# Optimization experiments

Hardware: AMD Instinct MI355X
Metric: run time of the kernel (lower is better)

Reference implementation:

```python
import jax, jax.numpy as jnp
import numpy as np

B, T, C, H, HD = 2, 2048, 1024, 16, 64
EPS = 1e-6

def rmsnorm(x):
    return x * jax.lax.rsqrt(jnp.mean(x * x, axis=-1, keepdims=True) + EPS)

def rotary_cos_sin(seq_len, hd):
    inv_freq = 1.0 / (10000.0 ** (jnp.arange(0, hd, 2, dtype=jnp.float32) / hd))
    freqs = jnp.arange(seq_len, dtype=jnp.float32)[:, None] * inv_freq[None, :]  # [T, hd/2]
    return jnp.cos(freqs)[None, :, None, :], jnp.sin(freqs)[None, :, None, :]

def apply_rotary(x, cos, sin):
    x1, x2 = x[..., : HD // 2], x[..., HD // 2 :]
    return jnp.concatenate([x1 * cos + x2 * sin, -x1 * sin + x2 * cos], axis=-1)


def setup_inputs() -> dict:
    key = jax.random.key(0)
    ks = jax.random.split(key, 8)
    return {
        "x": jax.random.normal(ks[0], (B, T, C), jnp.float32),
        "w_qkv": jax.random.normal(ks[1], (3 * C, C), jnp.float32) * 0.02,
        "w_out": jax.random.normal(ks[2], (C, C), jnp.float32) * 0.02,
        "hyp_curvature": jax.random.uniform(ks[3], (1, H, 1, 1), jnp.float32, 0.5, 1.5),
        "w_uv": jax.random.normal(ks[4], (8 * C, C), jnp.float32) * 0.02,
        "b_uv": jnp.zeros((8 * C,), jnp.float32),
        "w_mlp_out": jax.random.normal(ks[5], (C, 4 * C), jnp.float32) * 0.02,
        "b_mlp_out": jnp.zeros((C,), jnp.float32),
    }


def reference(x, w_qkv, w_out, hyp_curvature, w_uv, b_uv, w_mlp_out, b_mlp_out):
    # --- pre-norm (euc/hyp branch uses rms_norm) ---
    h = rmsnorm(x)
    # --- QKV projection ---
    qkv = h @ w_qkv.T  # [B,T,3C]
    q, k, v = jnp.split(qkv, 3, axis=-1)
    q = q.reshape(B, T, H, HD)
    k = k.reshape(B, T, H, HD)
    v = v.reshape(B, T, H, HD)
    # --- RoPE ---
    cos, sin = rotary_cos_sin(T, HD)
    q = apply_rotary(q, cos, sin)
    k = apply_rotary(k, cos, sin)
    # [B,H,T,HD]
    q = jnp.transpose(q, (0, 2, 1, 3))
    k = jnp.transpose(k, (0, 2, 1, 3))
    v = jnp.transpose(v, (0, 2, 1, 3))
    # --- hyperbolic (Lorentz) attention ---
    kc = hyp_curvature  # [1,H,1,1], positive per-head curvature
    q0 = jnp.sqrt(kc + jnp.sum(q * q, axis=-1, keepdims=True))  # time coord [B,H,T,1]
    k0 = jnp.sqrt(kc + jnp.sum(k * k, axis=-1, keepdims=True))
    # Lorentz inner product <u,v>_L = -u0*v0 + u.v  -> [B,H,T,S]
    lorentz = jnp.einsum("bhtd,bhsd->bhts", q, k) - q0 * jnp.swapaxes(k0, -1, -2)
    dis = jnp.sqrt(kc) * jnp.arccosh(jnp.maximum(-lorentz / kc, 1.0 + EPS))
    causal = jnp.tril(jnp.ones((T, T), dtype=bool))
    scores = jnp.where(causal, -dis, -jnp.inf)  # hyp_attn_weight='neg_dis'
    attn_w = jax.nn.softmax(scores, axis=-1)
    attn = jnp.einsum("bhts,bhsd->bhtd", attn_w, v)
    attn = jnp.transpose(attn, (0, 2, 1, 3)).reshape(B, T, C)
    x = x + attn @ w_out.T
    # --- SwiGLU MLP with pre rms_norm ---
    h = rmsnorm(x)
    uv = h @ w_uv.T + b_uv
    u, vg = jnp.split(uv, 2, axis=-1)
    h_mlp = (u * jax.nn.silu(vg)) @ w_mlp_out.T + b_mlp_out
    return x + h_mlp
```

## Files before the change

kernel.cpp:

```cpp
#include <hip/hip_runtime.h>
#include <cstdint>
#include <cmath>

typedef __bf16 bf16;
typedef __attribute__((ext_vector_type(8))) __bf16 bf16x8;
typedef __attribute__((ext_vector_type(4))) __bf16 bf16x4;
typedef __attribute__((ext_vector_type(2))) __bf16 bf16x2;
typedef __attribute__((ext_vector_type(4))) float f32x4;

constexpr int B_ = 2, T_ = 2048, C_ = 1024, H_ = 16, HD_ = 64;
constexpr int M_ = B_ * T_;

#define EXP2F(x) __builtin_amdgcn_exp2f(x)
#define LOG2F(x) __builtin_amdgcn_logf(x)
#define SQRTF(x) __builtin_amdgcn_sqrtf(x)
#define RCPF(x)  __builtin_amdgcn_rcpf(x)

__device__ __forceinline__ void gld16(const void* g, void* l) {
  __builtin_amdgcn_global_load_lds((const __attribute__((address_space(1))) void*)g,
                                   (__attribute__((address_space(3))) void*)l, 16, 0, 0);
}

__global__ __launch_bounds__(256) void cast_all_kernel(const float* __restrict__ s0,
                                                       const float* __restrict__ s1,
                                                       const float* __restrict__ s2,
                                                       const float* __restrict__ s3,
                                                       const float* __restrict__ s4,
                                                       bf16* __restrict__ d0,
                                                       bf16* __restrict__ d1,
                                                       bf16* __restrict__ d2,
                                                       bf16* __restrict__ d3,
                                                       float* __restrict__ d4) {
  size_t gid = (size_t)blockIdx.x * 256 + threadIdx.x;
  if (gid >= 786432 + 262144 + 2097152 + 1048576) {
    size_t g4 = gid - (786432 + 262144 + 2097152 + 1048576);
    if (g4 >= 2048) return;
    int r = (int)(g4 * 4);
    int dr;
    if (r < 4096) { int blk = r >> 6, i = r & 63; dr = blk * 128 + i; }
    else { int j = r - 4096; int blk = j >> 6, i = j & 63; dr = blk * 128 + 64 + i; }
    *(f32x4*)(d4 + dr) = *(const f32x4*)(s4 + r);
    return;
  }
  const float* src;
  bf16* dst;
  size_t dstoff;
  if (gid < 786432) { src = s0; dst = d0; dstoff = gid * 4; }
  else if (gid < 786432 + 262144) { gid -= 786432; src = s1; dst = d1; dstoff = gid * 4; }
  else if (gid < 786432 + 262144 + 2097152) {
    gid -= 786432 + 262144; src = s2; dst = d2;
    size_t elem = gid * 4;
    int r = (int)(elem >> 10), c = (int)(elem & 1023);
    int dr;
    if (r < 4096) { int blk = r >> 6, i = r & 63; dr = blk * 128 + i; }
    else { int j = r - 4096; int blk = j >> 6, i = j & 63; dr = blk * 128 + 64 + i; }
    dstoff = ((size_t)dr << 10) | (size_t)c;
  }
  else { gid -= 786432 + 262144 + 2097152; src = s3; dst = d3; dstoff = gid * 4; }
  f32x4 v = *(const f32x4*)(src + gid * 4);
  bf16x4 o;
  o[0] = (bf16)v[0]; o[1] = (bf16)v[1]; o[2] = (bf16)v[2]; o[3] = (bf16)v[3];
  *(bf16x4*)(dst + dstoff) = o;
}

template <int MODE, typename OutT>
__global__ __launch_bounds__(256) void gemm_bt(const bf16* __restrict__ A,
                                               const bf16* __restrict__ Bw,
                                               OutT* __restrict__ Cmat,
                                               const float* __restrict__ bias,
                                               const float* __restrict__ R,
                                               int M, int N, int K, int lda) {
  __shared__ __align__(16) bf16 shmem[4 * 128 * 32];
  bf16* const AlsH[2] = { &shmem[0], &shmem[4096] };
  bf16* const BlsH[2] = { &shmem[2 * 4096], &shmem[3 * 4096] };
  const int tid  = threadIdx.x;
  const int wave = tid >> 6;
  const int lane = tid & 63;
  const int quad = lane >> 4;
  const int l16  = lane & 15;
  const int bm = blockIdx.x * 128;
  const int bn = blockIdx.y * 128;
  const int wm = (wave & 1) * 64;
  const int wn = (wave >> 1) * 64;
  const int wn2 = (wave >> 1) * 32;
  const int srow   = lane >> 2;
  const int schunk = lane & 3;

  f32x4 acc[4][4];
#pragma unroll
  for (int i = 0; i < 4; i++)
#pragma unroll
    for (int j = 0; j < 4; j++) acc[i][j] = f32x4{0.f, 0.f, 0.f, 0.f};

  const bf16* Ag = A  + (size_t)(bm + wave * 32 + srow) * lda + schunk * 8;
  const bf16* Bg = Bw + (size_t)(bn + wave * 32 + srow) * K   + schunk * 8;
  bf16* AlsW0 = AlsH[0] + (wave * 32) * 32;
  bf16* AlsW1 = AlsH[1] + (wave * 32) * 32;
  bf16* BlsW0 = BlsH[0] + (wave * 32) * 32;
  bf16* BlsW1 = BlsH[1] + (wave * 32) * 32;

  for (int k0 = 0; k0 < K; k0 += 64) {
    gld16(Ag + k0,                         AlsW0);
    gld16(Ag + k0 + (size_t)16 * lda,      AlsW0 + 16 * 32);
    gld16(Ag + k0 + 32,                    AlsW1);
    gld16(Ag + k0 + 32 + (size_t)16 * lda, AlsW1 + 16 * 32);
    gld16(Bg + k0,                         BlsW0);
    gld16(Bg + k0 + (size_t)16 * K,        BlsW0 + 16 * 32);
    gld16(Bg + k0 + 32,                    BlsW1);
    gld16(Bg + k0 + 32 + (size_t)16 * K,   BlsW1 + 16 * 32);
    __syncthreads();

#pragma unroll
    for (int hh = 0; hh < 2; hh++) {
      bf16x8 af[4], bfr[4];
#pragma unroll
      for (int mt = 0; mt < 4; mt++)
        af[mt] = *(const bf16x8*)&AlsH[hh][(wm + mt * 16 + l16) * 32 + quad * 8];
#pragma unroll
      for (int nt = 0; nt < 4; nt++) {
        const int cb = (MODE == 4)
                         ? ((nt < 2) ? (wn2 + nt * 16) : (64 + wn2 + (nt - 2) * 16))
                         : (wn + nt * 16);
        bfr[nt] = *(const bf16x8*)&BlsH[hh][(cb + l16) * 32 + quad * 8];
      }
#pragma unroll
      for (int mt = 0; mt < 4; mt++)
#pragma unroll
        for (int nt = 0; nt < 4; nt++)
          acc[mt][nt] = __builtin_amdgcn_mfma_f32_16x16x32_bf16(af[mt], bfr[nt], acc[mt][nt], 0, 0, 0);
    }
    __syncthreads();
  }

  if (MODE != 4) {
#pragma unroll
    for (int mt = 0; mt < 4; mt++) {
      const int row = bm + wm + mt * 16 + quad * 4;
#pragma unroll
      for (int nt = 0; nt < 4; nt++) {
        const int col = bn + wn + nt * 16 + l16;
        float bval = 0.f;
        if (MODE & 2) bval = bias[col];
#pragma unroll
        for (int r = 0; r < 4; r++) {
          float v = acc[mt][nt][r] + bval;
          if (MODE & 1) v += R[(size_t)(row + r) * N + col];
          Cmat[(size_t)(row + r) * N + col] = (OutT)v;
        }
      }
    }
  } else {
    const int colg0 = (bn >> 1) + wn2;
#pragma unroll
    for (int mt = 0; mt < 4; mt++) {
      const int row = bm + wm + mt * 16 + quad * 4;
#pragma unroll
      for (int ntl = 0; ntl < 2; ntl++) {
        const float bu = bias[bn + wn2 + ntl * 16 + l16];
        const float bv = bias[bn + 64 + wn2 + ntl * 16 + l16];
        const int col = colg0 + ntl * 16 + l16;
#pragma unroll
        for (int r = 0; r < 4; r++) {
          float u = acc[mt][ntl][r] + bu;
          float v = acc[mt][ntl + 2][r] + bv;
          float sig = RCPF(1.f + EXP2F(-v * 1.44269504f));
          Cmat[(size_t)(row + r) * N + col] = (OutT)(u * v * sig);
        }
      }
    }
  }
}

__global__ __launch_bounds__(256) void rmsnorm_kernel(const float* __restrict__ X,
                                                      bf16* __restrict__ O) {
  const int row = blockIdx.x;
  const int tid = threadIdx.x;
  const int wave = tid >> 6;
  f32x4 v = *(const f32x4*)(X + (size_t)row * C_ + tid * 4);
  float s = v[0] * v[0] + v[1] * v[1] + v[2] * v[2] + v[3] * v[3];
#pragma unroll
  for (int off = 32; off >= 1; off >>= 1) s += __shfl_xor(s, off);
  __shared__ float wsum[4];
  __shared__ float scale_sh;
  if ((tid & 63) == 0) wsum[wave] = s;
  __syncthreads();
  if (tid == 0)
    scale_sh = rsqrtf((wsum[0] + wsum[1] + wsum[2] + wsum[3]) * (1.f / (float)C_) + 1e-6f);
  __syncthreads();
  const float sc = scale_sh;
  bf16x4 o;
  o[0] = (bf16)(v[0] * sc); o[1] = (bf16)(v[1] * sc);
  o[2] = (bf16)(v[2] * sc); o[3] = (bf16)(v[3] * sc);
  *(bf16x4*)(O + (size_t)row * C_ + tid * 4) = o;
}

__global__ __launch_bounds__(256) void rotary_kernel(bf16* __restrict__ qkv,
                                                     const float* __restrict__ kcb,
                                                     float* __restrict__ q0b,
                                                     float* __restrict__ k0b) {
  const int wid  = blockIdx.x * 4 + (threadIdx.x >> 6);
  const int lane = threadIdx.x & 63;
  const int b = wid >> 15;
  const int rem = wid & 32767;
  const int t = rem >> 4;
  const int h = rem & 15;
  const int i = lane & 31;
  const float invf = expf(-((float)i / 32.f) * 9.210340371976184f);
  const float ang = (float)t * invf;
  const float cx = cosf(ang), sx = sinf(ang);
  const float kc = kcb[h];
  bf16* qp = qkv + (size_t)(b * T_ + t) * 3072 + h * 64;

#pragma unroll
  for (int which = 0; which < 2; which++) {
    bf16* p = qp + which * 1024;
    float x1 = (float)p[i];
    float x2 = (float)p[i + 32];
    float o = (lane < 32) ? (x1 * cx + x2 * sx) : (x2 * cx - x1 * sx);
    float ss = o * o;
#pragma unroll
    for (int off = 32; off >= 1; off >>= 1) ss += __shfl_xor(ss, off);
    p[lane] = (bf16)o;
    if (lane == 0) {
      float* dst = which == 0 ? q0b : k0b;
      dst[(size_t)(b * H_ + h) * T_ + t] = SQRTF(kc + ss);
    }
  }
}

__global__ __launch_bounds__(256) void attn_kernel(const bf16* __restrict__ qkv,
                                                   const float* __restrict__ q0b,
                                                   const float* __restrict__ k0b,
                                                   const float* __restrict__ kcb,
                                                   bf16* __restrict__ outp) {
  __shared__ __align__(16) bf16 Kls[2][64][72];
  __shared__ __align__(16) bf16 Vt[2][64][68];
  __shared__ __align__(16) bf16 Pls[4][16 * 36];
  __shared__ float k0s[2][64];

  const int tid = threadIdx.x;
  const int wave = tid >> 6, lane = tid & 63;
  const int quad = lane >> 4, l16 = lane & 15;
  const int bh = blockIdx.x;
  const int b = bh >> 4, h = bh & 15;

  const float kc = kcb[h];
  const float inv_kc = 1.f / kc;
  const float sqkc = SQRTF(kc);
  const int sp = tid & 31, dq = tid >> 5;
  bf16* Pl = Pls[wave];
  const float* q0base = q0b + (size_t)(b * H_ + h) * T_;
  const float* k0base = k0b + (size_t)(b * H_ + h) * T_;

  const int ty = 31 - (int)blockIdx.y;
  const int t0 = ty * 64;
  const int tb = t0 + wave * 16;
  const int nIter = ty + 1;

  const bf16* qrow = qkv + (size_t)(b * T_ + tb + l16) * 3072 + h * 64;
  bf16x8 aq0 = *(const bf16x8*)(qrow + quad * 8);
  bf16x8 aq1 = *(const bf16x8*)(qrow + 32 + quad * 8);
  float q0r[4];
#pragma unroll
  for (int r = 0; r < 4; r++) q0r[r] = q0base[tb + quad * 4 + r];

  f32x4 o[4];
#pragma unroll
  for (int dt = 0; dt < 4; dt++) o[dt] = f32x4{0.f, 0.f, 0.f, 0.f};
  float lrow[4] = {0.f, 0.f, 0.f, 0.f};

  const bf16* kvbase = qkv + (size_t)b * T_ * 3072 + 1024 + h * 64 + dq * 8;
  bf16x8 kv_a = *(const bf16x8*)(kvbase + (size_t)(2 * sp) * 3072);
  bf16x8 kv_b = *(const bf16x8*)(kvbase + (size_t)(2 * sp + 1) * 3072);
  bf16x8 vv_a = *(const bf16x8*)(kvbase + (size_t)(2 * sp) * 3072 + 1024);
  bf16x8 vv_b = *(const bf16x8*)(kvbase + (size_t)(2 * sp + 1) * 3072 + 1024);
  float k0v = (tid < 64) ? k0base[tid] : 0.f;

  for (int it = 0; it < nIter; ++it) {
    const int s0 = it * 64;
    const int buf = it & 1;
    *(bf16x8*)&Kls[buf][2 * sp][dq * 8]     = kv_a;
    *(bf16x8*)&Kls[buf][2 * sp + 1][dq * 8] = kv_b;
#pragma unroll
    for (int i2 = 0; i2 < 8; i2++) {
      bf16x2 pr;
      pr[0] = vv_a[i2];
      pr[1] = vv_b[i2];
      *(bf16x2*)&Vt[buf][dq * 8 + i2][2 * sp] = pr;
    }
    if (tid < 64) k0s[buf][tid] = k0v;
    __syncthreads();

    const int s0n = (it + 1 < nIter) ? s0 + 64 : s0;
    kv_a = *(const bf16x8*)(kvbase + (size_t)(s0n + 2 * sp) * 3072);
    kv_b = *(const bf16x8*)(kvbase + (size_t)(s0n + 2 * sp + 1) * 3072);
    vv_a = *(const bf16x8*)(kvbase + (size_t)(s0n + 2 * sp) * 3072 + 1024);
    vv_b = *(const bf16x8*)(kvbase + (size_t)(s0n + 2 * sp + 1) * 3072 + 1024);
    if (tid < 64) k0v = k0base[s0n + tid];

    f32x4 sc[4];
#pragma unroll
    for (int nt = 0; nt < 4; nt++) {
      sc[nt] = f32x4{0.f, 0.f, 0.f, 0.f};
      bf16x8 b0 = *(const bf16x8*)&Kls[buf][nt * 16 + l16][quad * 8];
      bf16x8 b1 = *(const bf16x8*)&Kls[buf][nt * 16 + l16][32 + quad * 8];
      sc[nt] = __builtin_amdgcn_mfma_f32_16x16x32_bf16(aq0, b0, sc[nt], 0, 0, 0);
      sc[nt] = __builtin_amdgcn_mfma_f32_16x16x32_bf16(aq1, b1, sc[nt], 0, 0, 0);
    }

    bf16x8 ap[2];
#pragma unroll
    for (int ck = 0; ck < 2; ck++) {
#pragma unroll
      for (int ntl = 0; ntl < 2; ntl++) {
        const int nt = ck * 2 + ntl;
        const float k0c = k0s[buf][nt * 16 + l16];
        const int s = s0 + nt * 16 + l16;
#pragma unroll
        for (int r = 0; r < 4; r++) {
          const int t = tb + quad * 4 + r;
          float lor = sc[nt][r] - q0r[r] * k0c;
          float ratio = fmaxf(-lor * inv_kc, 1.f + 1e-6f);
          float wv = ratio + SQRTF(ratio * ratio - 1.f);
          float p = EXP2F(-sqkc * LOG2F(wv));
          p = (s <= t) ? p : 0.f;
          lrow[r] += p;
          Pl[(quad * 4 + r) * 36 + ntl * 16 + l16] = (bf16)p;
        }
      }
      ap[ck] = *(const bf16x8*)&Pl[l16 * 36 + quad * 8];
    }
#pragma unroll
    for (int dt = 0; dt < 4; dt++) {
      bf16x8 bv0 = *(const bf16x8*)&Vt[buf][dt * 16 + l16][quad * 8];
      bf16x8 bv1 = *(const bf16x8*)&Vt[buf][dt * 16 + l16][32 + quad * 8];
      o[dt] = __builtin_amdgcn_mfma_f32_16x16x32_bf16(ap[0], bv0, o[dt], 0, 0, 0);
      o[dt] = __builtin_amdgcn_mfma_f32_16x16x32_bf16(ap[1], bv1, o[dt], 0, 0, 0);
    }
  }

#pragma unroll
  for (int r = 0; r < 4; r++) {
#pragma unroll
    for (int off = 1; off <= 8; off <<= 1) lrow[r] += __shfl_xor(lrow[r], off);
  }
#pragma unroll
  for (int r = 0; r < 4; r++) {
    const float invl = RCPF(lrow[r]);
    const int t = tb + quad * 4 + r;
#pragma unroll
    for (int dt = 0; dt < 4; dt++) {
      float val = o[dt][r] * invl;
      outp[(size_t)(b * T_ + t) * C_ + h * 64 + dt * 16 + l16] = (bf16)val;
    }
  }
}

extern "C" void kernel_launch(void* const* d_in, const int* in_sizes, int n_in,
                              void* d_out, int out_size, void* d_ws, size_t ws_size,
                              hipStream_t stream) {
  const float* x      = (const float*)d_in[0];
  const float* w_qkv  = (const float*)d_in[1];
  const float* w_out  = (const float*)d_in[2];
  const float* kcb    = (const float*)d_in[3];
  const float* w_uv   = (const float*)d_in[4];
  const float* b_uv   = (const float*)d_in[5];
  const float* w_mlp  = (const float*)d_in[6];
  const float* b_mlp  = (const float*)d_in[7];
  float* out = (float*)d_out;

  const size_t MB = 1024ull * 1024ull;
  char* w = (char*)d_ws;
  bf16*  wqkv_b  = (bf16*)(w + 0);
  bf16*  wout_b  = (bf16*)(w + 6 * MB);
  bf16*  wuv_p   = (bf16*)(w + 8 * MB);
  bf16*  wmlp_b  = (bf16*)(w + 24 * MB);
  bf16*  hbuf    = (bf16*)(w + 32 * MB);
  bf16*  qkvbuf  = (bf16*)(w + 40 * MB);
  bf16*  attnbuf = (bf16*)(w + 64 * MB);
  bf16*  gbuf    = (bf16*)(w + 40 * MB);
  float* x2buf   = (float*)(w + 72 * MB);
  float* q0b     = (float*)(w + 88 * MB);
  float* k0b     = (float*)(w + 88 * MB + 256 * 1024);
  float* biasp   = (float*)(w + 88 * MB + 512 * 1024);

  const int total4 = 786432 + 262144 + 2097152 + 1048576 + 2048;
  cast_all_kernel<<<(total4 + 255) / 256, 256, 0, stream>>>(
      w_qkv, w_out, w_uv, w_mlp, b_uv, wqkv_b, wout_b, wuv_p, wmlp_b, biasp);

  rmsnorm_kernel<<<M_, 256, 0, stream>>>(x, hbuf);
  gemm_bt<0, bf16><<<dim3(M_ / 128, 3072 / 128), 256, 0, stream>>>(
      hbuf, wqkv_b, qkvbuf, nullptr, nullptr, M_, 3072, 1024, 1024);
  rotary_kernel<<<(B_ * T_ * H_) / 4, 256, 0, stream>>>(qkvbuf, kcb, q0b, k0b);
  attn_kernel<<<dim3(B_ * H_, 32), 256, 0, stream>>>(qkvbuf, q0b, k0b, kcb, attnbuf);
  gemm_bt<1, float><<<dim3(M_ / 128, 1024 / 128), 256, 0, stream>>>(
      attnbuf, wout_b, x2buf, nullptr, x, M_, 1024, 1024, 1024);
  rmsnorm_kernel<<<M_, 256, 0, stream>>>(x2buf, hbuf);
  gemm_bt<4, bf16><<<dim3(M_ / 128, 8192 / 128), 256, 0, stream>>>(
      hbuf, wuv_p, gbuf, biasp, nullptr, M_, 4096, 1024, 1024);
  gemm_bt<3, float><<<dim3(M_ / 128, 1024 / 128), 256, 0, stream>>>(
      gbuf, wmlp_b, out, b_mlp, x2buf, M_, 1024, 4096, 4096);
}
```

Baseline: 437.7 us.

## Use 512-thread attention blocks with split K/V loaders and smaller GEMM M-tiles

```diff
diff --git a/kernel.cpp b/kernel.cpp
--- a/kernel.cpp
+++ b/kernel.cpp
@@ -63,58 +63,59 @@
   *(bf16x4*)(dst + dstoff) = o;
 }
 
-template <int MODE, typename OutT>
+template <int MODE, typename OutT, int BM = 128>
 __global__ __launch_bounds__(256) void gemm_bt(const bf16* __restrict__ A,
                                                const bf16* __restrict__ Bw,
                                                OutT* __restrict__ Cmat,
                                                const float* __restrict__ bias,
                                                const float* __restrict__ R,
                                                int M, int N, int K, int lda) {
-  __shared__ __align__(16) bf16 shmem[4 * 128 * 32];
-  bf16* const AlsH[2] = { &shmem[0], &shmem[4096] };
-  bf16* const BlsH[2] = { &shmem[2 * 4096], &shmem[3 * 4096] };
+  __shared__ __align__(16) bf16 shmem[(2 * BM + 2 * 128) * 32];
+  bf16* const AlsH[2] = { &shmem[0], &shmem[BM * 32] };
+  bf16* const BlsH[2] = { &shmem[2 * BM * 32], &shmem[2 * BM * 32 + 4096] };
   const int tid  = threadIdx.x;
   const int wave = tid >> 6;
   const int lane = tid & 63;
   const int quad = lane >> 4;
   const int l16  = lane & 15;
-  const int bm = blockIdx.x * 128;
+  const int bm = blockIdx.x * BM;
   const int bn = blockIdx.y * 128;
-  const int wm = (wave & 1) * 64;
+  const int wm = (wave & 1) * (BM / 2);
   const int wn = (wave >> 1) * 64;
   const int wn2 = (wave >> 1) * 32;
   const int srow   = lane >> 2;
   const int schunk = lane & 3;
-
-  f32x4 acc[4][4];
-#pragma unroll
-  for (int i = 0; i < 4; i++)
+  constexpr int MT = BM / 32;
+
+  f32x4 acc[MT][4];
+#pragma unroll
+  for (int i = 0; i < MT; i++)
 #pragma unroll
     for (int j = 0; j < 4; j++) acc[i][j] = f32x4{0.f, 0.f, 0.f, 0.f};
 
-  const bf16* Ag = A  + (size_t)(bm + wave * 32 + srow) * lda + schunk * 8;
+  const bf16* Ag = A  + (size_t)(bm + wave * (BM / 4) + srow) * lda + schunk * 8;
   const bf16* Bg = Bw + (size_t)(bn + wave * 32 + srow) * K   + schunk * 8;
-  bf16* AlsW0 = AlsH[0] + (wave * 32) * 32;
-  bf16* AlsW1 = AlsH[1] + (wave * 32) * 32;
+  bf16* AlsW0 = AlsH[0] + (wave * (BM / 4)) * 32;
+  bf16* AlsW1 = AlsH[1] + (wave * (BM / 4)) * 32;
   bf16* BlsW0 = BlsH[0] + (wave * 32) * 32;
   bf16* BlsW1 = BlsH[1] + (wave * 32) * 32;
 
   for (int k0 = 0; k0 < K; k0 += 64) {
-    gld16(Ag + k0,                         AlsW0);
-    gld16(Ag + k0 + (size_t)16 * lda,      AlsW0 + 16 * 32);
-    gld16(Ag + k0 + 32,                    AlsW1);
-    gld16(Ag + k0 + 32 + (size_t)16 * lda, AlsW1 + 16 * 32);
-    gld16(Bg + k0,                         BlsW0);
-    gld16(Bg + k0 + (size_t)16 * K,        BlsW0 + 16 * 32);
-    gld16(Bg + k0 + 32,                    BlsW1);
-    gld16(Bg + k0 + 32 + (size_t)16 * K,   BlsW1 + 16 * 32);
+    gld16(Ag + k0, AlsW0);
+    if (BM == 128) gld16(Ag + k0 + (size_t)16 * lda, AlsW0 + 16 * 32);
+    gld16(Ag + k0 + 32, AlsW1);
+    if (BM == 128) gld16(Ag + k0 + 32 + (size_t)16 * lda, AlsW1 + 16 * 32);
+    gld16(Bg + k0,                       BlsW0);
+    gld16(Bg + k0 + (size_t)16 * K,      BlsW0 + 16 * 32);
+    gld16(Bg + k0 + 32,                  BlsW1);
+    gld16(Bg + k0 + 32 + (size_t)16 * K, BlsW1 + 16 * 32);
     __syncthreads();
 
 #pragma unroll
     for (int hh = 0; hh < 2; hh++) {
-      bf16x8 af[4], bfr[4];
-#pragma unroll
-      for (int mt = 0; mt < 4; mt++)
+      bf16x8 af[MT], bfr[4];
+#pragma unroll
+      for (int mt = 0; mt < MT; mt++)
         af[mt] = *(const bf16x8*)&AlsH[hh][(wm + mt * 16 + l16) * 32 + quad * 8];
 #pragma unroll
       for (int nt = 0; nt < 4; nt++) {
@@ -124,7 +125,7 @@
         bfr[nt] = *(const bf16x8*)&BlsH[hh][(cb + l16) * 32 + quad * 8];
       }
 #pragma unroll
-      for (int mt = 0; mt < 4; mt++)
+      for (int mt = 0; mt < MT; mt++)
 #pragma unroll
         for (int nt = 0; nt < 4; nt++)
           acc[mt][nt] = __builtin_amdgcn_mfma_f32_16x16x32_bf16(af[mt], bfr[nt], acc[mt][nt], 0, 0, 0);
@@ -134,7 +135,7 @@
 
   if (MODE != 4) {
 #pragma unroll
-    for (int mt = 0; mt < 4; mt++) {
+    for (int mt = 0; mt < MT; mt++) {
       const int row = bm + wm + mt * 16 + quad * 4;
 #pragma unroll
       for (int nt = 0; nt < 4; nt++) {
@@ -152,7 +153,7 @@
   } else {
     const int colg0 = (bn >> 1) + wn2;
 #pragma unroll
-    for (int mt = 0; mt < 4; mt++) {
+    for (int mt = 0; mt < MT; mt++) {
       const int row = bm + wm + mt * 16 + quad * 4;
 #pragma unroll
       for (int ntl = 0; ntl < 2; ntl++) {
@@ -228,14 +229,14 @@
   }
 }
 
-__global__ __launch_bounds__(256) void attn_kernel(const bf16* __restrict__ qkv,
+__global__ __launch_bounds__(512) void attn_kernel(const bf16* __restrict__ qkv,
                                                    const float* __restrict__ q0b,
                                                    const float* __restrict__ k0b,
                                                    const float* __restrict__ kcb,
                                                    bf16* __restrict__ outp) {
   __shared__ __align__(16) bf16 Kls[2][64][72];
   __shared__ __align__(16) bf16 Vt[2][64][68];
-  __shared__ __align__(16) bf16 Pls[4][16 * 36];
+  __shared__ __align__(16) bf16 Pls[8][16 * 36];
   __shared__ float k0s[2][64];
 
   const int tid = threadIdx.x;
@@ -247,15 +248,17 @@
   const float kc = kcb[h];
   const float inv_kc = 1.f / kc;
   const float sqkc = SQRTF(kc);
-  const int sp = tid & 31, dq = tid >> 5;
+  const int role = tid >> 8;
+  const int st = tid & 255;
+  const int sp = st & 31, dq = st >> 5;
   bf16* Pl = Pls[wave];
   const float* q0base = q0b + (size_t)(b * H_ + h) * T_;
   const float* k0base = k0b + (size_t)(b * H_ + h) * T_;
 
-  const int ty = 31 - (int)blockIdx.y;
-  const int t0 = ty * 64;
+  const int ty = 15 - (int)blockIdx.y;
+  const int t0 = ty * 128;
   const int tb = t0 + wave * 16;
-  const int nIter = ty + 1;
+  const int nIter = 2 * ty + 2;
 
   const bf16* qrow = qkv + (size_t)(b * T_ + tb + l16) * 3072 + h * 64;
   bf16x8 aq0 = *(const bf16x8*)(qrow + quad * 8);
@@ -269,73 +272,74 @@
   for (int dt = 0; dt < 4; dt++) o[dt] = f32x4{0.f, 0.f, 0.f, 0.f};
   float lrow[4] = {0.f, 0.f, 0.f, 0.f};
 
-  const bf16* kvbase = qkv + (size_t)b * T_ * 3072 + 1024 + h * 64 + dq * 8;
-  bf16x8 kv_a = *(const bf16x8*)(kvbase + (size_t)(2 * sp) * 3072);
-  bf16x8 kv_b = *(const bf16x8*)(kvbase + (size_t)(2 * sp + 1) * 3072);
-  bf16x8 vv_a = *(const bf16x8*)(kvbase + (size_t)(2 * sp) * 3072 + 1024);
-  bf16x8 vv_b = *(const bf16x8*)(kvbase + (size_t)(2 * sp + 1) * 3072 + 1024);
+  const bf16* base = qkv + (size_t)b * T_ * 3072 + 1024 + role * 1024 + h * 64 + dq * 8;
+  bf16x8 pf_a = *(const bf16x8*)(base + (size_t)(2 * sp) * 3072);
+  bf16x8 pf_b = *(const bf16x8*)(base + (size_t)(2 * sp + 1) * 3072);
   float k0v = (tid < 64) ? k0base[tid] : 0.f;
 
   for (int it = 0; it < nIter; ++it) {
     const int s0 = it * 64;
     const int buf = it & 1;
-    *(bf16x8*)&Kls[buf][2 * sp][dq * 8]     = kv_a;
-    *(bf16x8*)&Kls[buf][2 * sp + 1][dq * 8] = kv_b;
-#pragma unroll
-    for (int i2 = 0; i2 < 8; i2++) {
-      bf16x2 pr;
-      pr[0] = vv_a[i2];
-      pr[1] = vv_b[i2];
-      *(bf16x2*)&Vt[buf][dq * 8 + i2][2 * sp] = pr;
+    if (role == 0) {
+      *(bf16x8*)&Kls[buf][2 * sp][dq * 8]     = pf_a;
+      *(bf16x8*)&Kls[buf][2 * sp + 1][dq * 8] = pf_b;
+    } else {
+#pragma unroll
+      for (int i2 = 0; i2 < 8; i2++) {
+        bf16x2 pr;
+        pr[0] = pf_a[i2];
+        pr[1] = pf_b[i2];
+        *(bf16x2*)&Vt[buf][dq * 8 + i2][2 * sp] = pr;
+      }
     }
     if (tid < 64) k0s[buf][tid] = k0v;
     __syncthreads();
 
     const int s0n = (it + 1 < nIter) ? s0 + 64 : s0;
-    kv_a = *(const bf16x8*)(kvbase + (size_t)(s0n + 2 * sp) * 3072);
-    kv_b = *(const bf16x8*)(kvbase + (size_t)(s0n + 2 * sp + 1) * 3072);
-    vv_a = *(const bf16x8*)(kvbase + (size_t)(s0n + 2 * sp) * 3072 + 1024);
-    vv_b = *(const bf16x8*)(kvbase + (size_t)(s0n + 2 * sp + 1) * 3072 + 1024);
+    pf_a = *(const bf16x8*)(base + (size_t)(s0n + 2 * sp) * 3072);
+    pf_b = *(const bf16x8*)(base + (size_t)(s0n + 2 * sp + 1) * 3072);
     if (tid < 64) k0v = k0base[s0n + tid];
 
-    f32x4 sc[4];
-#pragma unroll
-    for (int nt = 0; nt < 4; nt++) {
-      sc[nt] = f32x4{0.f, 0.f, 0.f, 0.f};
-      bf16x8 b0 = *(const bf16x8*)&Kls[buf][nt * 16 + l16][quad * 8];
-      bf16x8 b1 = *(const bf16x8*)&Kls[buf][nt * 16 + l16][32 + quad * 8];
-      sc[nt] = __builtin_amdgcn_mfma_f32_16x16x32_bf16(aq0, b0, sc[nt], 0, 0, 0);
-      sc[nt] = __builtin_amdgcn_mfma_f32_16x16x32_bf16(aq1, b1, sc[nt], 0, 0, 0);
-    }
-
-    bf16x8 ap[2];
-#pragma unroll
-    for (int ck = 0; ck < 2; ck++) {
-#pragma unroll
-      for (int ntl = 0; ntl < 2; ntl++) {
-        const int nt = ck * 2 + ntl;
-        const float k0c = k0s[buf][nt * 16 + l16];
-        const int s = s0 + nt * 16 + l16;
-#pragma unroll
-        for (int r = 0; r < 4; r++) {
-          const int t = tb + quad * 4 + r;
-          float lor = sc[nt][r] - q0r[r] * k0c;
-          float ratio = fmaxf(-lor * inv_kc, 1.f + 1e-6f);
-          float wv = ratio + SQRTF(ratio * ratio - 1.f);
-          float p = EXP2F(-sqkc * LOG2F(wv));
-          p = (s <= t) ? p : 0.f;
-          lrow[r] += p;
-          Pl[(quad * 4 + r) * 36 + ntl * 16 + l16] = (bf16)p;
+    if (s0 <= tb + 15) {
+      f32x4 sc[4];
+#pragma unroll
+      for (int nt = 0; nt < 4; nt++) {
+        sc[nt] = f32x4{0.f, 0.f, 0.f, 0.f};
+        bf16x8 b0 = *(const bf16x8*)&Kls[buf][nt * 16 + l16][quad * 8];
+        bf16x8 b1 = *(const bf16x8*)&Kls[buf][nt * 16 + l16][32 + quad * 8];
+        sc[nt] = __builtin_amdgcn_mfma_f32_16x16x32_bf16(aq0, b0, sc[nt], 0, 0, 0);
+        sc[nt] = __builtin_amdgcn_mfma_f32_16x16x32_bf16(aq1, b1, sc[nt], 0, 0, 0);
+      }
+
+      bf16x8 ap[2];
+#pragma unroll
+      for (int ck = 0; ck < 2; ck++) {
+#pragma unroll
+        for (int ntl = 0; ntl < 2; ntl++) {
+          const int nt = ck * 2 + ntl;
+          const float k0c = k0s[buf][nt * 16 + l16];
+          const int s = s0 + nt * 16 + l16;
+#pragma unroll
+          for (int r = 0; r < 4; r++) {
+            const int t = tb + quad * 4 + r;
+            float lor = sc[nt][r] - q0r[r] * k0c;
+            float ratio = fmaxf(-lor * inv_kc, 1.f + 1e-6f);
+            float wv = ratio + SQRTF(ratio * ratio - 1.f);
+            float p = EXP2F(-sqkc * LOG2F(wv));
+            p = (s <= t) ? p : 0.f;
+            lrow[r] += p;
+            Pl[(quad * 4 + r) * 36 + ntl * 16 + l16] = (bf16)p;
+          }
         }
-      }
-      ap[ck] = *(const bf16x8*)&Pl[l16 * 36 + quad * 8];
-    }
-#pragma unroll
-    for (int dt = 0; dt < 4; dt++) {
-      bf16x8 bv0 = *(const bf16x8*)&Vt[buf][dt * 16 + l16][quad * 8];
-      bf16x8 bv1 = *(const bf16x8*)&Vt[buf][dt * 16 + l16][32 + quad * 8];
-      o[dt] = __builtin_amdgcn_mfma_f32_16x16x32_bf16(ap[0], bv0, o[dt], 0, 0, 0);
-      o[dt] = __builtin_amdgcn_mfma_f32_16x16x32_bf16(ap[1], bv1, o[dt], 0, 0, 0);
+        ap[ck] = *(const bf16x8*)&Pl[l16 * 36 + quad * 8];
+      }
+#pragma unroll
+      for (int dt = 0; dt < 4; dt++) {
+        bf16x8 bv0 = *(const bf16x8*)&Vt[buf][dt * 16 + l16][quad * 8];
+        bf16x8 bv1 = *(const bf16x8*)&Vt[buf][dt * 16 + l16][32 + quad * 8];
+        o[dt] = __builtin_amdgcn_mfma_f32_16x16x32_bf16(ap[0], bv0, o[dt], 0, 0, 0);
+        o[dt] = __builtin_amdgcn_mfma_f32_16x16x32_bf16(ap[1], bv1, o[dt], 0, 0, 0);
+      }
     }
   }
 
@@ -392,12 +396,12 @@
   gemm_bt<0, bf16><<<dim3(M_ / 128, 3072 / 128), 256, 0, stream>>>(
       hbuf, wqkv_b, qkvbuf, nullptr, nullptr, M_, 3072, 1024, 1024);
   rotary_kernel<<<(B_ * T_ * H_) / 4, 256, 0, stream>>>(qkvbuf, kcb, q0b, k0b);
-  attn_kernel<<<dim3(B_ * H_, 32), 256, 0, stream>>>(qkvbuf, q0b, k0b, kcb, attnbuf);
-  gemm_bt<1, float><<<dim3(M_ / 128, 1024 / 128), 256, 0, stream>>>(
+  attn_kernel<<<dim3(B_ * H_, 16), 512, 0, stream>>>(qkvbuf, q0b, k0b, kcb, attnbuf);
+  gemm_bt<1, float, 64><<<dim3(M_ / 64, 1024 / 128), 256, 0, stream>>>(
       attnbuf, wout_b, x2buf, nullptr, x, M_, 1024, 1024, 1024);
   rmsnorm_kernel<<<M_, 256, 0, stream>>>(x2buf, hbuf);
   gemm_bt<4, bf16><<<dim3(M_ / 128, 8192 / 128), 256, 0, stream>>>(
       hbuf, wuv_p, gbuf, biasp, nullptr, M_, 4096, 1024, 1024);
-  gemm_bt<3, float><<<dim3(M_ / 128, 1024 / 128), 256, 0, stream>>>(
+  gemm_bt<3, float, 64><<<dim3(M_ / 64, 1024 / 128), 256, 0, stream>>>(
       gbuf, wmlp_b, out, b_mlp, x2buf, M_, 1024, 4096, 4096);
 }
```

After: 416.3 us. 4.9% less time.
